# Performance work log

Measured on AMD Instinct MI355X. Metric: run time of the kernel, lower is better.

The kernel has to match this reference:

```python
import jax, jax.numpy as jnp
import numpy as np

N_NODES = 100000
N_EDGES = 1600000
IN_DIM = 128
HID = 64
OUT_DIM = 3


def _glorot(key, shape):
    fan_in, fan_out = shape[0], shape[1]
    std = (2.0 / (fan_in + fan_out)) ** 0.5
    return jax.random.normal(key, shape, jnp.float32) * std


def setup_inputs() -> dict:
    key = jax.random.key(0)
    ks = jax.random.split(key, 12)
    x = jax.random.normal(ks[0], (N_NODES, IN_DIM), jnp.float32)
    edge_index = jax.random.randint(ks[1], (2, N_EDGES), 0, N_NODES, dtype=jnp.int32)
    return {
        "x": x,
        "edge_index": edge_index,
        "W1": _glorot(ks[2], (IN_DIM, HID)), "b1": jnp.zeros((HID,), jnp.float32),
        "W2": _glorot(ks[3], (HID, HID)), "b2": jnp.zeros((HID,), jnp.float32),
        "W3": _glorot(ks[4], (HID, HID)), "b3": jnp.zeros((HID,), jnp.float32),
        "W4": _glorot(ks[5], (HID, HID // 2)), "b4": jnp.zeros((HID // 2,), jnp.float32),
        "Wh": _glorot(ks[6], (HID // 2, OUT_DIM)), "bh": jnp.zeros((OUT_DIM,), jnp.float32),
    }


def reference(x, edge_index, W1, b1, W2, b2, W3, b3, W4, b4, Wh, bh):
    n = x.shape[0]
    self_loops = jnp.arange(n, dtype=edge_index.dtype)
    src = jnp.concatenate([edge_index[0], self_loops])  # message sources j
    dst = jnp.concatenate([edge_index[1], self_loops])  # aggregation targets i
    # symmetric GCN normalization with self-loops: deg over targets (unit edge weights)
    deg = jax.ops.segment_sum(jnp.ones_like(dst, jnp.float32), dst, num_segments=n)
    dinv = jnp.where(deg > 0, jax.lax.rsqrt(deg), 0.0)
    norm = dinv[src] * dinv[dst]  # [E+N]

    def gcn(h, W, b):
        h = h @ W  # transform first (PyG GCNConv order)
        agg = jax.ops.segment_sum(h[src] * norm[:, None], dst, num_segments=n)
        return agg + b

    h = jax.nn.relu(gcn(x, W1, b1))   # dropout is identity in eval mode
    h = jax.nn.relu(gcn(h, W2, b2))
    h = jax.nn.relu(gcn(h, W3, b3))
    h = jax.nn.relu(gcn(h, W4, b4))
    return h @ Wh + bh  # [N, 3]
```

## Files before the change

kernel.cpp:

```cpp
#include <hip/hip_runtime.h>
#include <hip/hip_bf16.h>
#include <hip/hip_fp16.h>
#include <cstdint>


#define MAXD 512
#define EB   8192
#define PADSLACK 2048

typedef _Float16 half8v __attribute__((ext_vector_type(8)));
typedef _Float16 half2v __attribute__((ext_vector_type(2)));
typedef float    float4v __attribute__((ext_vector_type(4)));

#if defined(__has_builtin)
#if __has_builtin(__builtin_amdgcn_fdot2)
#define HAVE_FDOT2 1
#endif
#endif

__device__ __forceinline__ float fdot2f(half2v a, half2v b, float c) {
#ifdef HAVE_FDOT2
    return __builtin_amdgcn_fdot2(a, b, c, false);
#else
    return c + (float)a[0] * (float)b[0] + (float)a[1] * (float)b[1];
#endif
}

__device__ __forceinline__ void digit_base_scan(const int* __restrict__ totals,
                                                int ND, int* pairs, int* cbs) {
    const int t = threadIdx.x;
    const int e0 = 2 * t, e1 = 2 * t + 1;
    int v0 = (e0 < ND) ? totals[e0] : 0;
    int v1 = (e1 < ND) ? totals[e1] : 0;
    pairs[t] = v0 + v1;
    __syncthreads();
    for (int off = 1; off < 256; off <<= 1) {
        int x = (t >= off) ? pairs[t - off] : 0;
        __syncthreads();
        pairs[t] += x;
        __syncthreads();
    }
    int ep = pairs[t] - v0 - v1;
    cbs[e0] = ep;
    cbs[e1] = ep + v0;
    __syncthreads();
}

__device__ __forceinline__ void hist_body(const int* __restrict__ ei,
                                          int* __restrict__ histM, int E, int b) {
    __shared__ int hist[MAXD];
    const int tid = threadIdx.x;
    hist[tid] = 0; hist[tid + 256] = 0;
    __syncthreads();
    const int base = b * EB;
#pragma unroll 2
    for (int it = 0; it < EB / 256; it += 4) {
        int d[4]; bool ok[4];
#pragma unroll
        for (int u = 0; u < 4; ++u) {
            int e = base + (it + u) * 256 + tid;
            ok[u] = e < E;
            d[u] = ok[u] ? ei[E + e] : 0;
        }
#pragma unroll
        for (int u = 0; u < 4; ++u)
            if (ok[u]) atomicAdd(&hist[d[u] >> 8], 1);
    }
    __syncthreads();
    histM[(size_t)b * MAXD + tid] = hist[tid];
    histM[(size_t)b * MAXD + tid + 256] = hist[tid + 256];
}

__global__ __launch_bounds__(256) void scan_digits_k(int* __restrict__ histM,
                                                     int* __restrict__ totals,
                                                     int NBLK) {
    __shared__ int s[256];
    const int t = threadIdx.x, dg = blockIdx.x;
    int v = (t < NBLK) ? histM[(size_t)t * MAXD + dg] : 0;
    s[t] = v;
    __syncthreads();
    for (int off = 1; off < 256; off <<= 1) {
        int x = (t >= off) ? s[t - off] : 0;
        __syncthreads();
        s[t] += x;
        __syncthreads();
    }
    if (t < NBLK) histM[(size_t)t * MAXD + dg] = s[t] - v;
    if (t == 255) totals[dg] = s[255];
}

__device__ __forceinline__ void gemm1_mfma_body(const float* __restrict__ X,
                                                const float* __restrict__ W,
                                                __half* __restrict__ Aout,
                                                int n, int bx) {
    __shared__ _Float16 WT[64][136];
    const int t = threadIdx.x;
#pragma unroll
    for (int p = 0; p < 8; ++p) {
        int f4 = t + p * 256;
        int k  = f4 >> 4;
        int o  = (f4 & 15) * 4;
        float4 v = reinterpret_cast<const float4*>(W)[f4];
        WT[o + 0][k] = (_Float16)v.x;
        WT[o + 1][k] = (_Float16)v.y;
        WT[o + 2][k] = (_Float16)v.z;
        WT[o + 3][k] = (_Float16)v.w;
    }
    __syncthreads();

    const int lane = t & 63;
    const int wv   = t >> 6;
    const int m16  = lane & 15;
    const int quad = lane >> 4;
    const int r0   = bx * 64 + wv * 16;
    int ra = r0 + m16; if (ra >= n) ra = n - 1;

    const float4* xrow = reinterpret_cast<const float4*>(X + (size_t)ra * 128);
    half8v a[4];
#pragma unroll
    for (int h = 0; h < 4; ++h) {
        int f0 = (h * 32 + quad * 8) >> 2;
        float4 v0 = xrow[f0];
        float4 v1 = xrow[f0 + 1];
        a[h][0] = (_Float16)v0.x; a[h][1] = (_Float16)v0.y;
        a[h][2] = (_Float16)v0.z; a[h][3] = (_Float16)v0.w;
        a[h][4] = (_Float16)v1.x; a[h][5] = (_Float16)v1.y;
        a[h][6] = (_Float16)v1.z; a[h][7] = (_Float16)v1.w;
    }
#pragma unroll
    for (int tt = 0; tt < 4; ++tt) {
        const half8v* wt = reinterpret_cast<const half8v*>(&WT[tt * 16 + m16][0]);
        float4v z = {0.f, 0.f, 0.f, 0.f};
#pragma unroll
        for (int h = 0; h < 4; ++h)
            z = __builtin_amdgcn_mfma_f32_16x16x32_f16(a[h], wt[h * 4 + quad], z, 0, 0, 0);
#pragma unroll
        for (int reg = 0; reg < 4; ++reg) {
            int row = r0 + quad * 4 + reg;
            if (row < n)
                Aout[(size_t)row * 64 + tt * 16 + m16] = __float2half_rn(z[reg]);
        }
    }
}

__device__ __forceinline__ void pack_body(const int* __restrict__ ei,
                                          const int* __restrict__ histM,
                                          const int* __restrict__ totals,
                                          int* __restrict__ packed,
                                          int E, int ND, int b) {
    __shared__ int pairs[256];
    __shared__ int cbs[MAXD];
    __shared__ int cur[MAXD];
    const int tid = threadIdx.x;
    digit_base_scan(totals, ND, pairs, cbs);
    for (int t = tid; t < ND; t += 256)
        cur[t] = cbs[t] + histM[(size_t)b * MAXD + t];
    __syncthreads();
    const int base = b * EB;
    for (int it = 0; it < EB / 256; it += 4) {
        int s[4], d[4]; bool ok[4];
#pragma unroll
        for (int u = 0; u < 4; ++u) {
            int e = base + (it + u) * 256 + tid;
            ok[u] = e < E;
            if (ok[u]) { s[u] = ei[e]; d[u] = ei[E + e]; }
        }
#pragma unroll
        for (int u = 0; u < 4; ++u) {
            if (ok[u]) {
                int pos = atomicAdd(&cur[d[u] >> 8], 1);
                packed[pos] = (s[u] << 8) | (d[u] & 255);
            }
        }
    }
}

__global__ __launch_bounds__(256) void hist_gemm1_k(
    const int* __restrict__ ei, int* __restrict__ histM, int E,
    const float* __restrict__ x, const float* __restrict__ W1,
    __half* __restrict__ A1, int n, int NH) {
    const int bx = blockIdx.x;
    if (bx < NH) hist_body(ei, histM, E, bx);
    else         gemm1_mfma_body(x, W1, A1, n, bx - NH);
}

__global__ __launch_bounds__(256) void pack_gemm1_k(
    const int* __restrict__ ei, const int* __restrict__ histM,
    const int* __restrict__ totals, int* __restrict__ packed,
    const float* __restrict__ x, const float* __restrict__ W1,
    __half* __restrict__ A1, int n, int E, int ND, int NPB, int G1) {
    const int bx = blockIdx.x;
    if (bx < NPB) pack_body(ei, histM, totals, packed, E, ND, bx);
    else          gemm1_mfma_body(x, W1, A1, n, G1 + bx - NPB);
}

__global__ __launch_bounds__(256) void bucket_k(const int* __restrict__ packed,
                                                const int* __restrict__ totals,
                                                int ND,
                                                int* __restrict__ col,
                                                int4* __restrict__ rpc,
                                                float* __restrict__ dinv,
                                                const __half* __restrict__ Araw,
                                                __half* __restrict__ Th, int n) {
    __shared__ int   pairs[256];
    __shared__ int   cbs[MAXD];
    __shared__ int   hist[256];
    __shared__ int   pref[256];
    __shared__ int   cur[256];
    __shared__ float dinv_l[256];

    const int tid = threadIdx.x;
    const int dg  = blockIdx.x;
    digit_base_scan(totals, ND, pairs, cbs);
    const int base  = cbs[dg];
    const int m     = totals[dg];
    const int basep = base + dg * PADSLACK;

    hist[tid] = 0;
    __syncthreads();
    for (int k0 = 0; k0 < m; k0 += 1024) {
        int v[4]; bool ok[4];
#pragma unroll
        for (int u = 0; u < 4; ++u) {
            int k = k0 + u * 256 + tid;
            ok[u] = k < m;
            v[u] = ok[u] ? packed[base + k] : 0;
        }
#pragma unroll
        for (int u = 0; u < 4; ++u)
            if (ok[u]) atomicAdd(&hist[v[u] & 255], 1);
    }
    __syncthreads();
    const int deg   = hist[tid];
    const int cnt_p = (deg + 8) & ~7;
    pref[tid] = cnt_p;
    __syncthreads();
    for (int off = 1; off < 256; off <<= 1) {
        int x = (tid >= off) ? pref[tid - off] : 0;
        __syncthreads();
        pref[tid] += x;
        __syncthreads();
    }
    const int rp = basep + pref[tid] - cnt_p;
    const float di = rsqrtf((float)(deg + 1));
    dinv_l[tid] = di;
    cur[tid] = rp + 1;
    const int d = dg * 256 + tid;
    if (d < n) {
        rpc[d]  = make_int4(rp, cnt_p, __float_as_int(di), 0);
        dinv[d] = di;
        col[rp] = d;
        for (int k = deg + 1; k < cnt_p; ++k) col[rp + k] = n;
    }
    __syncthreads();
    for (int k0 = 0; k0 < m; k0 += 1024) {
        int v[4]; bool ok[4];
#pragma unroll
        for (int u = 0; u < 4; ++u) {
            int k = k0 + u * 256 + tid;
            ok[u] = k < m;
            v[u] = ok[u] ? packed[base + k] : 0;
        }
#pragma unroll
        for (int u = 0; u < 4; ++u) {
            if (ok[u]) {
                int pos = atomicAdd(&cur[v[u] & 255], 1);
                col[pos] = v[u] >> 8;
            }
        }
    }
    const int r0 = dg * 256;
#pragma unroll 4
    for (int it = 0; it < 16; ++it) {
        int idx = it * 256 + tid;
        int rl  = idx >> 4;
        int r   = r0 + rl;
        if (r < n) {
            union { uint2 u; __half h[4]; } iv;
            iv.u = reinterpret_cast<const uint2*>(Araw)[(size_t)r * 16 + (idx & 15)];
            float dd = dinv_l[rl];
            union { ushort4 u; __half h[4]; } pk;
            pk.h[0] = __float2half_rn(__half2float(iv.h[0]) * dd);
            pk.h[1] = __float2half_rn(__half2float(iv.h[1]) * dd);
            pk.h[2] = __float2half_rn(__half2float(iv.h[2]) * dd);
            pk.h[3] = __float2half_rn(__half2float(iv.h[3]) * dd);
            reinterpret_cast<ushort4*>(Th)[(size_t)r * 16 + (idx & 15)] = pk.u;
        }
    }
    if (dg == 0 && tid < 16) {
        uint2 z; z.x = 0u; z.y = 0u;
        reinterpret_cast<uint2*>(Th)[(size_t)n * 16 + tid] = z;
    }
}

template <int OUT>
__global__ __launch_bounds__(256) void gemm_mfma_k(
    const _Float16* __restrict__ H, const float* __restrict__ W,
    const float* __restrict__ dinv, _Float16* __restrict__ T, int n) {
    constexpr int NT = OUT / 16;
    const int lane = threadIdx.x & 63;
    const int m16  = lane & 15;
    const int quad = lane >> 4;
    const int wid  = (blockIdx.x * blockDim.x + threadIdx.x) >> 6;
    const int nw   = (gridDim.x * blockDim.x) >> 6;

    half8v bfrag[NT][2];
#pragma unroll
    for (int t = 0; t < NT; ++t)
#pragma unroll
        for (int h = 0; h < 2; ++h)
#pragma unroll
            for (int j = 0; j < 8; ++j)
                bfrag[t][h][j] = (_Float16)W[(size_t)(h * 32 + quad * 8 + j) * OUT
                                             + t * 16 + m16];

    const int nblk = (n + 15) >> 4;
    for (int rb = wid; rb < nblk; rb += nw) {
        const int r0 = rb * 16;
        int ra = r0 + m16; if (ra >= n) ra = n - 1;
        const half8v* hrow = reinterpret_cast<const half8v*>(H + (size_t)ra * 64);
        half8v a0 = hrow[quad];
        half8v a1 = hrow[4 + quad];

        float4v dfr[NT];
#pragma unroll
        for (int t = 0; t < NT; ++t) {
            float4v z = {0.f, 0.f, 0.f, 0.f};
            z = __builtin_amdgcn_mfma_f32_16x16x32_f16(a0, bfrag[t][0], z, 0, 0, 0);
            z = __builtin_amdgcn_mfma_f32_16x16x32_f16(a1, bfrag[t][1], z, 0, 0, 0);
            dfr[t] = z;
        }
#pragma unroll
        for (int reg = 0; reg < 4; ++reg) {
            int row = r0 + quad * 4 + reg;
            if (row < n) {
                float di = dinv[row];
#pragma unroll
                for (int t = 0; t < NT; ++t)
                    T[(size_t)row * 64 + t * 16 + m16] =
                        (_Float16)(dfr[t][reg] * di);
            }
        }
    }
}

template <int NB, int LR>
__device__ __forceinline__ void gather_batch(int c_l, const uint2* __restrict__ T2,
                                             int q, int sw, float4& acc) {
    constexpr int NSW = 64 / LR;
    constexpr int GPE = 8 / NSW;
    constexpr int NV  = NB * GPE;
    const half2v s10 = {(_Float16)1.f, (_Float16)0.f};
    const half2v s01 = {(_Float16)0.f, (_Float16)1.f};
    uint2 v[NV];
#pragma unroll
    for (int g = 0; g < NB; ++g)
#pragma unroll
        for (int u = 0; u < GPE; ++u) {
            int cc = __shfl(c_l, g * 8 + u * NSW + sw, 64);
            v[g * GPE + u] = T2[(size_t)cc * 16 + q];
        }
#pragma unroll
    for (int k = 0; k < NV; ++k) {
        union { uint2 uu; half2v h[2]; } cv; cv.uu = v[k];
        acc.x = fdot2f(cv.h[0], s10, acc.x);
        acc.y = fdot2f(cv.h[0], s01, acc.y);
        acc.z = fdot2f(cv.h[1], s10, acc.z);
        acc.w = fdot2f(cv.h[1], s01, acc.w);
    }
}

template <int LR, bool FUSE_HEAD>
__global__ __launch_bounds__(256, 8) void agg_k(const __half* __restrict__ T,
                                             const int4* __restrict__ rpc,
                                             const int* __restrict__ col,
                                             const float* __restrict__ bias,
                                             void* __restrict__ O, int n,
                                             const float* __restrict__ Wh,
                                             const float* __restrict__ bh) {
    constexpr int NSW = 64 / LR;
    constexpr int GPE = 8 / NSW;
    const int lane = threadIdx.x & 63;
    const int q    = lane % LR;
    const int sw   = lane / LR;
    const int wid  = (blockIdx.x * blockDim.x + threadIdx.x) >> 6;
    const int nw   = (gridDim.x * blockDim.x) >> 6;
    if (wid >= n) return;

    const uint2* __restrict__ T2 = reinterpret_cast<const uint2*>(T);
    const float4 b4 = reinterpret_cast<const float4*>(bias)[q];

    int ib = wid + nw; if (ib >= n) ib = n - 1;
    int4 rc_a = rpc[wid];
    int4 rc_b = rpc[ib];
    int  c_a  = col[rc_a.x + lane];

    for (int i = wid; i < n; i += nw) {
        int ic = i + 2 * nw; if (ic >= n) ic = n - 1;
        int4 rc_c = rpc[ic];
        int  c_nx = col[rc_b.x + lane];

        const int   cnt   = rc_a.y;
        const int   start = rc_a.x;
        const float di    = __int_as_float(rc_a.z);

        float4 acc = make_float4(0.f, 0.f, 0.f, 0.f);
        if (cnt <= 64) {
            switch (cnt >> 3) {
                case 1: gather_batch<1, LR>(c_a, T2, q, sw, acc); break;
                case 2: gather_batch<2, LR>(c_a, T2, q, sw, acc); break;
                case 3: gather_batch<3, LR>(c_a, T2, q, sw, acc); break;
                case 4: gather_batch<4, LR>(c_a, T2, q, sw, acc); break;
                case 5: gather_batch<5, LR>(c_a, T2, q, sw, acc); break;
                case 6: gather_batch<6, LR>(c_a, T2, q, sw, acc); break;
                case 7: gather_batch<7, LR>(c_a, T2, q, sw, acc); break;
                default: gather_batch<8, LR>(c_a, T2, q, sw, acc); break;
            }
        } else {
            const half2v s10 = {(_Float16)1.f, (_Float16)0.f};
            const half2v s01 = {(_Float16)0.f, (_Float16)1.f};
            for (int base = 0; base < cnt; base += 64) {
                const int m = min(64, cnt - base);
                int c_l = col[start + base + lane];
                for (int jg = 0; jg < m; jg += 8) {
                    int cc[GPE]; uint2 v[GPE];
#pragma unroll
                    for (int u = 0; u < GPE; ++u)
                        cc[u] = __shfl(c_l, jg + u * NSW + sw, 64);
#pragma unroll
                    for (int u = 0; u < GPE; ++u) v[u] = T2[(size_t)cc[u] * 16 + q];
#pragma unroll
                    for (int u = 0; u < GPE; ++u) {
                        union { uint2 uu; half2v h[2]; } cv; cv.uu = v[u];
                        acc.x = fdot2f(cv.h[0], s10, acc.x);
                        acc.y = fdot2f(cv.h[0], s01, acc.y);
                        acc.z = fdot2f(cv.h[1], s10, acc.z);
                        acc.w = fdot2f(cv.h[1], s01, acc.w);
                    }
                }
            }
        }
#pragma unroll
        for (int off = LR; off < 64; off <<= 1) {
            acc.x += __shfl_xor(acc.x, off, 64);
            acc.y += __shfl_xor(acc.y, off, 64);
            acc.z += __shfl_xor(acc.z, off, 64);
            acc.w += __shfl_xor(acc.w, off, 64);
        }
        float4 h;
        h.x = fmaxf(fmaf(di, acc.x, b4.x), 0.f);
        h.y = fmaxf(fmaf(di, acc.y, b4.y), 0.f);
        h.z = fmaxf(fmaf(di, acc.z, b4.z), 0.f);
        h.w = fmaxf(fmaf(di, acc.w, b4.w), 0.f);
        if constexpr (!FUSE_HEAD) {
            if (sw == 0) {
                union { ushort4 u; __half hh[4]; } pk;
                pk.hh[0] = __float2half_rn(h.x);
                pk.hh[1] = __float2half_rn(h.y);
                pk.hh[2] = __float2half_rn(h.z);
                pk.hh[3] = __float2half_rn(h.w);
                ushort* base_p = (ushort*)O + (size_t)i * 64;
                *reinterpret_cast<ushort4*>(base_p + 4 * q) = pk.u;
            }
        } else {
            float* Of = (float*)O;
            float p0 = h.x * Wh[(4 * q + 0) * 3 + 0];
            float p1 = h.x * Wh[(4 * q + 0) * 3 + 1];
            float p2 = h.x * Wh[(4 * q + 0) * 3 + 2];
            p0 = fmaf(h.y, Wh[(4 * q + 1) * 3 + 0], p0);
            p1 = fmaf(h.y, Wh[(4 * q + 1) * 3 + 1], p1);
            p2 = fmaf(h.y, Wh[(4 * q + 1) * 3 + 2], p2);
            p0 = fmaf(h.z, Wh[(4 * q + 2) * 3 + 0], p0);
            p1 = fmaf(h.z, Wh[(4 * q + 2) * 3 + 1], p1);
            p2 = fmaf(h.z, Wh[(4 * q + 2) * 3 + 2], p2);
            p0 = fmaf(h.w, Wh[(4 * q + 3) * 3 + 0], p0);
            p1 = fmaf(h.w, Wh[(4 * q + 3) * 3 + 1], p1);
            p2 = fmaf(h.w, Wh[(4 * q + 3) * 3 + 2], p2);
#pragma unroll
            for (int off = 1; off < LR; off <<= 1) {
                p0 += __shfl_xor(p0, off, 64);
                p1 += __shfl_xor(p1, off, 64);
                p2 += __shfl_xor(p2, off, 64);
            }
            if (lane == 0) {
                Of[(size_t)i * 3 + 0] = p0 + bh[0];
                Of[(size_t)i * 3 + 1] = p1 + bh[1];
                Of[(size_t)i * 3 + 2] = p2 + bh[2];
            }
        }
        rc_a = rc_b; rc_b = rc_c; c_a = c_nx;
    }
}

extern "C" void kernel_launch(void* const* d_in, const int* in_sizes, int n_in,
                              void* d_out, int out_size, void* d_ws, size_t ws_size,
                              hipStream_t stream) {
    const float* x  = (const float*)d_in[0];
    const int*   ei = (const int*)d_in[1];
    const float* W1 = (const float*)d_in[2];
    const float* b1 = (const float*)d_in[3];
    const float* W2 = (const float*)d_in[4];
    const float* b2 = (const float*)d_in[5];
    const float* W3 = (const float*)d_in[6];
    const float* b3 = (const float*)d_in[7];
    const float* W4 = (const float*)d_in[8];
    const float* b4 = (const float*)d_in[9];
    const float* Wh = (const float*)d_in[10];
    const float* bh = (const float*)d_in[11];
    float* out = (float*)d_out;

    const int n = in_sizes[0] / 128;
    const int E = in_sizes[1] / 2;
    const int ND   = (n + 255) / 256;
    const int NBLK = (E + EB - 1) / EB;

    char* ws = (char*)d_ws;
    auto alloc = [&](size_t bytes) {
        char* p = ws;
        ws += (bytes + 255) & ~(size_t)255;
        return p;
    };
    int*    histM  = (int*)alloc((size_t)NBLK * MAXD * 4);
    int*    totals = (int*)alloc((size_t)MAXD * 4);
    int*    packed = (int*)alloc((size_t)E * 4);
    int*    col    = (int*)alloc(((size_t)E + (size_t)ND * PADSLACK + 256) * 4);
    int4*   rpc    = (int4*)alloc((size_t)n * 16);
    float*  dinv   = (float*)alloc((size_t)n * 4);
    __half* bufA   = (__half*)alloc((size_t)n * 64 * 2);
    __half* bufH   = (__half*)alloc(((size_t)n + 1) * 64 * 2);
    __half* bufG   = bufA;

    dim3 blk(256);
    const int G  = (n + 63) / 64;
    const int G1 = G / 3;
    const int G2 = G - G1;
    const int agg_blocks = 2048;
    const int mfma_blocks = 640;

    hist_gemm1_k<<<dim3(NBLK + G1), blk, 0, stream>>>(ei, histM, E, x, W1, bufA, n, NBLK);
    scan_digits_k<<<dim3(ND), blk, 0, stream>>>(histM, totals, NBLK);
    pack_gemm1_k<<<dim3(NBLK + G2), blk, 0, stream>>>(ei, histM, totals, packed,
                                                      x, W1, bufA, n, E, ND, NBLK, G1);
    bucket_k<<<dim3(ND), blk, 0, stream>>>(packed, totals, ND, col, rpc,
                                           dinv, bufA, bufH, n);
    agg_k<16, false><<<dim3(agg_blocks), blk, 0, stream>>>(
        bufH, rpc, col, b1, bufG, n, nullptr, nullptr);
    gemm_mfma_k<64><<<dim3(mfma_blocks), blk, 0, stream>>>(
        (const _Float16*)bufG, W2, dinv, (_Float16*)bufH, n);
    agg_k<16, false><<<dim3(agg_blocks), blk, 0, stream>>>(
        bufH, rpc, col, b2, bufG, n, nullptr, nullptr);
    gemm_mfma_k<64><<<dim3(mfma_blocks), blk, 0, stream>>>(
        (const _Float16*)bufG, W3, dinv, (_Float16*)bufH, n);
    agg_k<16, false><<<dim3(agg_blocks), blk, 0, stream>>>(
        bufH, rpc, col, b3, bufG, n, nullptr, nullptr);
    gemm_mfma_k<32><<<dim3(mfma_blocks), blk, 0, stream>>>(
        (const _Float16*)bufG, W4, dinv, (_Float16*)bufH, n);
    agg_k<8, true><<<dim3(agg_blocks), blk, 0, stream>>>(
        bufH, rpc, col, b4, out, n, Wh, bh);
}
```

Measured before the change: 352.3 us.

## Pad CSR rows to multiples of 4 and stage GEMM1 output through LDS

Neighbor-list padding goes from multiples of 8 to multiples of 4, so fewer sentinel rows are gathered per node. A new tail path handles a trailing group of 4, pointing the unused lanes at the sentinel row. The long-row loop is rebuilt on top of the batched gather helper. Separately, GEMM1 results for full tiles are staged in shared memory and written out with coalesced 16-byte stores, adding an LDS buffer and some extra branching.

```diff
diff --git a/kernel.cpp b/kernel.cpp
--- a/kernel.cpp
+++ b/kernel.cpp
@@ -94,6 +94,7 @@
                                                 __half* __restrict__ Aout,
                                                 int n, int bx) {
     __shared__ _Float16 WT[64][136];
+    __shared__ _Float16 ST[4][1024];
     const int t = threadIdx.x;
 #pragma unroll
     for (int p = 0; p < 8; ++p) {
@@ -113,6 +114,7 @@
     const int m16  = lane & 15;
     const int quad = lane >> 4;
     const int r0   = bx * 64 + wv * 16;
+    const bool fastw = (r0 + 16 <= n);
     int ra = r0 + m16; if (ra >= n) ra = n - 1;
 
     const float4* xrow = reinterpret_cast<const float4*>(X + (size_t)ra * 128);
@@ -134,12 +136,24 @@
 #pragma unroll
         for (int h = 0; h < 4; ++h)
             z = __builtin_amdgcn_mfma_f32_16x16x32_f16(a[h], wt[h * 4 + quad], z, 0, 0, 0);
-#pragma unroll
-        for (int reg = 0; reg < 4; ++reg) {
-            int row = r0 + quad * 4 + reg;
-            if (row < n)
-                Aout[(size_t)row * 64 + tt * 16 + m16] = __float2half_rn(z[reg]);
-        }
+        if (fastw) {
+#pragma unroll
+            for (int reg = 0; reg < 4; ++reg)
+                ST[wv][(quad * 4 + reg) * 64 + tt * 16 + m16] = (_Float16)z[reg];
+        } else {
+#pragma unroll
+            for (int reg = 0; reg < 4; ++reg) {
+                int row = r0 + quad * 4 + reg;
+                if (row < n)
+                    Aout[(size_t)row * 64 + tt * 16 + m16] = __float2half_rn(z[reg]);
+            }
+        }
+    }
+    if (fastw) {
+        const uint4* st = reinterpret_cast<const uint4*>(&ST[wv][0]);
+        uint4* gp = reinterpret_cast<uint4*>((ushort*)Aout + (size_t)r0 * 64);
+        gp[lane]      = st[lane];
+        gp[lane + 64] = st[lane + 64];
     }
 }
 
@@ -232,7 +246,7 @@
     }
     __syncthreads();
     const int deg   = hist[tid];
-    const int cnt_p = (deg + 8) & ~7;
+    const int cnt_p = (deg + 4) & ~3;
     pref[tid] = cnt_p;
     __syncthreads();
     for (int off = 1; off < 256; off <<= 1) {
@@ -370,6 +384,27 @@
     }
 }
 
+template <int LR>
+__device__ __forceinline__ void gather_tail4(int c_l, const uint2* __restrict__ T2,
+                                             int q, int sw, float4& acc,
+                                             int g8, int nsent) {
+    const half2v s10 = {(_Float16)1.f, (_Float16)0.f};
+    const half2v s01 = {(_Float16)0.f, (_Float16)1.f};
+    int cc;
+    if constexpr (LR == 16) {
+        cc = __shfl(c_l, g8 * 8 + sw, 64);
+    } else {
+        cc = __shfl(c_l, g8 * 8 + (sw & 3), 64);
+        if (sw >= 4) cc = nsent;
+    }
+    uint2 v = T2[(size_t)cc * 16 + q];
+    union { uint2 uu; half2v h[2]; } cv; cv.uu = v;
+    acc.x = fdot2f(cv.h[0], s10, acc.x);
+    acc.y = fdot2f(cv.h[0], s01, acc.y);
+    acc.z = fdot2f(cv.h[1], s10, acc.z);
+    acc.w = fdot2f(cv.h[1], s01, acc.w);
+}
+
 template <int LR, bool FUSE_HEAD>
 __global__ __launch_bounds__(256, 8) void agg_k(const __half* __restrict__ T,
                                              const int4* __restrict__ rpc,
@@ -406,7 +441,9 @@
 
         float4 acc = make_float4(0.f, 0.f, 0.f, 0.f);
         if (cnt <= 64) {
-            switch (cnt >> 3) {
+            const int g8 = cnt >> 3;
+            switch (g8) {
+                case 0: break;
                 case 1: gather_batch<1, LR>(c_a, T2, q, sw, acc); break;
                 case 2: gather_batch<2, LR>(c_a, T2, q, sw, acc); break;
                 case 3: gather_batch<3, LR>(c_a, T2, q, sw, acc); break;
@@ -416,28 +453,28 @@
                 case 7: gather_batch<7, LR>(c_a, T2, q, sw, acc); break;
                 default: gather_batch<8, LR>(c_a, T2, q, sw, acc); break;
             }
+            if (cnt & 4) gather_tail4<LR>(c_a, T2, q, sw, acc, g8, n);
         } else {
-            const half2v s10 = {(_Float16)1.f, (_Float16)0.f};
-            const half2v s01 = {(_Float16)0.f, (_Float16)1.f};
-            for (int base = 0; base < cnt; base += 64) {
-                const int m = min(64, cnt - base);
+            int base = 0;
+            for (; base + 64 <= cnt; base += 64) {
                 int c_l = col[start + base + lane];
-                for (int jg = 0; jg < m; jg += 8) {
-                    int cc[GPE]; uint2 v[GPE];
-#pragma unroll
-                    for (int u = 0; u < GPE; ++u)
-                        cc[u] = __shfl(c_l, jg + u * NSW + sw, 64);
-#pragma unroll
-                    for (int u = 0; u < GPE; ++u) v[u] = T2[(size_t)cc[u] * 16 + q];
-#pragma unroll
-                    for (int u = 0; u < GPE; ++u) {
-                        union { uint2 uu; half2v h[2]; } cv; cv.uu = v[u];
-                        acc.x = fdot2f(cv.h[0], s10, acc.x);
-                        acc.y = fdot2f(cv.h[0], s01, acc.y);
-                        acc.z = fdot2f(cv.h[1], s10, acc.z);
-                        acc.w = fdot2f(cv.h[1], s01, acc.w);
-                    }
+                gather_batch<8, LR>(c_l, T2, q, sw, acc);
+            }
+            int rem = cnt - base;
+            if (rem) {
+                int c_l = col[start + base + lane];
+                const int g8 = rem >> 3;
+                switch (g8) {
+                    case 0: break;
+                    case 1: gather_batch<1, LR>(c_l, T2, q, sw, acc); break;
+                    case 2: gather_batch<2, LR>(c_l, T2, q, sw, acc); break;
+                    case 3: gather_batch<3, LR>(c_l, T2, q, sw, acc); break;
+                    case 4: gather_batch<4, LR>(c_l, T2, q, sw, acc); break;
+                    case 5: gather_batch<5, LR>(c_l, T2, q, sw, acc); break;
+                    case 6: gather_batch<6, LR>(c_l, T2, q, sw, acc); break;
+                    default: gather_batch<7, LR>(c_l, T2, q, sw, acc); break;
                 }
+                if (rem & 4) gather_tail4<LR>(c_l, T2, q, sw, acc, g8, n);
             }
         }
 #pragma unroll
```

Result: slower. 520.5 us (+47.7%).
